# Optimization experiments

Measured on AMD Instinct MI355X. Metric: run time of the kernel, lower is better.

The kernel has to match this reference:

```python
import jax, jax.numpy as jnp
import numpy as np

PALACE_N = 64   # base palace mask size
PALACE_BLOCK = 8  # 8 palaces of 8 positions each


def _palace_base():
    # base 64x64 mask: 1.0 within a palace (8x8 diagonal blocks), 0.5 across palaces
    pid = jnp.arange(PALACE_N) // PALACE_BLOCK
    intra = pid[:, None] == pid[None, :]
    return jnp.where(intra, 1.0, 0.5).astype(jnp.float32)


def _get_mask(T, inter_palace_weight):
    # tile base mask by index modulo 64 (matches mask[i % 64, j % 64])
    base = _palace_base()
    ii = jnp.arange(T) % PALACE_N
    base_T = base[ii[:, None], ii[None, :]]            # [T, T]
    intra = (base_T == 1.0).astype(jnp.float32)
    inter = (base_T < 1.0).astype(jnp.float32)
    return intra + jax.nn.sigmoid(inter_palace_weight) * inter


def setup_inputs() -> dict:
    key = jax.random.key(0)
    ks = jax.random.split(key, 5)
    B, T, D = 4, 2048, 1024
    x = jax.random.normal(ks[0], (B, T, D), dtype=jnp.float32)
    s = 1.0 / np.sqrt(D)
    Wq = jax.random.normal(ks[1], (D, D), dtype=jnp.float32) * s
    Wk = jax.random.normal(ks[2], (D, D), dtype=jnp.float32) * s
    Wv = jax.random.normal(ks[3], (D, D), dtype=jnp.float32) * s
    inter_palace_weight = jnp.float32(0.1)
    return {"x": x, "Wq": Wq, "Wk": Wk, "Wv": Wv,
            "inter_palace_weight": inter_palace_weight}


def reference(x, Wq, Wk, Wv, inter_palace_weight):
    B, T, D = x.shape
    H = 16
    hd = D // H
    scale = hd ** -0.5
    pmask = _get_mask(T, inter_palace_weight)          # [T, T]
    # torch Linear: x @ W.T
    q = (x @ Wq.T).reshape(B, T, H, hd)
    k = (x @ Wk.T).reshape(B, T, H, hd)
    v = (x @ Wv.T).reshape(B, T, H, hd)
    attn = jnp.einsum('bqhd,bkhd->bhqk', q, k) * scale
    attn = attn * pmask[None, None, :, :]
    attn = jax.nn.softmax(attn, axis=-1)
    attn = jnp.nan_to_num(attn, nan=0.0)
    out = jnp.einsum('bhqk,bkhd->bqhd', attn, v)
    return out.reshape(B, T, D)
```

## Files before the change

kernel.cpp:

```cpp
#include <hip/hip_runtime.h>

typedef unsigned short u16;
typedef unsigned int u32;
typedef short bf16x8 __attribute__((ext_vector_type(8)));
typedef float f32x4 __attribute__((ext_vector_type(4)));

#define AS_GLOBAL __attribute__((address_space(1)))
#define AS_LDS __attribute__((address_space(3)))

__device__ __forceinline__ void async16(const void* g, void* l) {
  __builtin_amdgcn_global_load_lds((const AS_GLOBAL u32*)g, (AS_LDS u32*)l, 16, 0, 0);
}

__device__ __forceinline__ u16 f2bf(float f) {
  u32 u = __builtin_bit_cast(u32, f);
  u += 0x7FFFu + ((u >> 16) & 1u);
  return (u16)(u >> 16);
}

__device__ __forceinline__ u32 pk2bf(float lo, float hi) {
  return __builtin_amdgcn_perm(__builtin_bit_cast(u32, hi),
                               __builtin_bit_cast(u32, lo), 0x07060302u);
}

__device__ __forceinline__ float fexp2(float x) {
#if __has_builtin(__builtin_amdgcn_exp2f)
  return __builtin_amdgcn_exp2f(x);
#else
  return exp2f(x);
#endif
}

__global__ __launch_bounds__(256) void cvt_all(const float* __restrict__ x,
                                               const float* __restrict__ wq,
                                               const float* __restrict__ wk,
                                               const float* __restrict__ wv,
                                               u16* __restrict__ xb,
                                               u16* __restrict__ wb) {
  const int blk = blockIdx.x;
  const float* src;
  u16* dst;
  int i;
  if (blk < 8192) {
    src = x; dst = xb; i = blk * 256 + threadIdx.x;
  } else if (blk < 9216) {
    src = wq; dst = wb; i = (blk - 8192) * 256 + threadIdx.x;
  } else if (blk < 10240) {
    src = wk; dst = wb + 1048576; i = (blk - 9216) * 256 + threadIdx.x;
  } else {
    src = wv; dst = wb + 2097152; i = (blk - 10240) * 256 + threadIdx.x;
  }
  float4 f = reinterpret_cast<const float4*>(src)[i];
  ushort4 o;
  o.x = f2bf(f.x); o.y = f2bf(f.y); o.z = f2bf(f.z); o.w = f2bf(f.w);
  reinterpret_cast<ushort4*>(dst)[i] = o;
}

__global__ __launch_bounds__(256, 3) void qkv_gemm(const u16* __restrict__ X,
                                                   const u16* __restrict__ W,
                                                   u16* __restrict__ O) {
  const int z = blockIdx.z;
  const u16* Wz = W + (size_t)z * (1024 * 1024);
  u16* Oz = O + (size_t)z * (8192 * 1024);

  __shared__ __align__(16) u16 As[2][128 * 32];
  __shared__ __align__(16) u16 Bs[2][128 * 32];

  const int t = threadIdx.x;
  const int lane = t & 63, w = t >> 6, quad = lane >> 4, lq = lane & 15;
  const int wm = (w >> 1) * 64, wn = (w & 1) * 64;
  const size_t m0 = (size_t)blockIdx.x * 128;
  const int n0 = blockIdx.y * 128;
  const int srow = t >> 2, sseg = (t & 3) * 8;

  f32x4 acc[4][4];
#pragma unroll
  for (int i = 0; i < 4; ++i)
#pragma unroll
    for (int j = 0; j < 4; ++j) acc[i][j] = f32x4{0.f, 0.f, 0.f, 0.f};

  const u16* ga = X + (m0 + srow) * 1024 + sseg;
  const u16* gb = Wz + (size_t)(n0 + srow) * 1024 + sseg;

  async16(ga, &As[0][srow * 32 + sseg]);
  async16(ga + 64 * 1024, &As[0][(64 + srow) * 32 + sseg]);
  async16(gb, &Bs[0][srow * 32 + sseg]);
  async16(gb + 64 * 1024, &Bs[0][(64 + srow) * 32 + sseg]);

  for (int kt = 0; kt < 32; ++kt) {
    const int cur = kt & 1;
    __syncthreads();
    if (kt < 31) {
      const int k1 = (kt + 1) * 32;
      async16(ga + k1, &As[cur ^ 1][srow * 32 + sseg]);
      async16(ga + 64 * 1024 + k1, &As[cur ^ 1][(64 + srow) * 32 + sseg]);
      async16(gb + k1, &Bs[cur ^ 1][srow * 32 + sseg]);
      async16(gb + 64 * 1024 + k1, &Bs[cur ^ 1][(64 + srow) * 32 + sseg]);
    }
    bf16x8 af[4], bfr[4];
#pragma unroll
    for (int i = 0; i < 4; ++i)
      af[i] = *reinterpret_cast<const bf16x8*>(&As[cur][(wm + i * 16 + lq) * 32 + quad * 8]);
#pragma unroll
    for (int j = 0; j < 4; ++j)
      bfr[j] = *reinterpret_cast<const bf16x8*>(&Bs[cur][(wn + j * 16 + lq) * 32 + quad * 8]);
#pragma unroll
    for (int i = 0; i < 4; ++i)
#pragma unroll
      for (int j = 0; j < 4; ++j)
        acc[i][j] = __builtin_amdgcn_mfma_f32_16x16x32_bf16(af[i], bfr[j], acc[i][j], 0, 0, 0);
  }

#pragma unroll
  for (int i = 0; i < 4; ++i) {
#pragma unroll
    for (int j = 0; j < 4; ++j) {
      const int n = n0 + wn + j * 16 + lq;
      const int hh = n >> 6, d = n & 63;
#pragma unroll
      for (int r = 0; r < 4; ++r) {
        const size_t m = m0 + wm + i * 16 + quad * 4 + r;
        const size_t bb = m >> 11, tt = m & 2047;
        if (z != 2)
          Oz[((bb * 16 + hh) * 2048 + tt) * 64 + d] = f2bf(acc[i][j][r]);
        else
          Oz[((bb * 16 + hh) * 64 + d) * 2048 + tt] = f2bf(acc[i][j][r]);
      }
    }
  }
}

__global__ __launch_bounds__(256, 4) void palace_attn(const u16* __restrict__ Q,
                                                      const u16* __restrict__ K,
                                                      const u16* __restrict__ Vt,
                                                      float* __restrict__ out,
                                                      const float* __restrict__ wptr) {
  const int bh = blockIdx.x, qt = blockIdx.y;
  const int h = bh & 15, b = bh >> 4;
  const size_t base = (size_t)bh * (2048 * 64);

  __shared__ __align__(16) u16 Ks[64 * 64];
  __shared__ __align__(16) u16 Vs[64 * 64];
  __shared__ __align__(16) u16 Ps[4][32 * 72];

  const int t = threadIdx.x;
  const int w = t >> 6, lane = t & 63, quad = lane >> 4, lq = lane & 15;
  const float sig = 1.f / (1.f + __expf(-wptr[0]));
  const float Ci = 0.125f * 1.44269504f;
  const float Co = Ci * sig;
  const float MC = 14.4269504f;

  float coef[2][4];
#pragma unroll
  for (int qg = 0; qg < 2; ++qg) {
    const int qp = (((w & 1) * 32) + qg * 16 + lq) >> 3;
#pragma unroll
    for (int kg = 0; kg < 4; ++kg)
      coef[qg][kg] = (qp == kg * 2 + (quad >> 1)) ? Ci : Co;
  }

  bf16x8 qf[2][2];
#pragma unroll
  for (int qg = 0; qg < 2; ++qg)
#pragma unroll
    for (int kc = 0; kc < 2; ++kc)
      qf[qg][kc] = *reinterpret_cast<const bf16x8*>(
          Q + base + (size_t)(qt * 128 + w * 32 + qg * 16 + lq) * 64 + kc * 32 + quad * 8);

  int ko[2], vo[2];
#pragma unroll
  for (int r = 0; r < 2; ++r) {
    const int slot = r * 256 + t;
    const int row = slot >> 3;
    const int cl = (slot & 7) ^ (row & 7);
    ko[r] = row * 64 + cl * 8;
    vo[r] = row * 2048 + cl * 8;
  }

  f32x4 O[2][4];
  float lsum[2] = {0.f, 0.f};
#pragma unroll
  for (int qg = 0; qg < 2; ++qg)
#pragma unroll
    for (int dg = 0; dg < 4; ++dg) O[qg][dg] = f32x4{0.f, 0.f, 0.f, 0.f};

  const int x7 = lq & 7;

  for (int kt = 0; kt < 32; ++kt) {
    const u16* kgp = K + base + (size_t)kt * 4096;
    const u16* vgp = Vt + base + (size_t)kt * 64;
    __syncthreads();
    async16(kgp + ko[0], &Ks[(w * 64) * 8]);
    async16(kgp + ko[1], &Ks[(256 + w * 64) * 8]);
    async16(vgp + vo[0], &Vs[(w * 64) * 8]);
    async16(vgp + vo[1], &Vs[(256 + w * 64) * 8]);
    __syncthreads();

    f32x4 s[4][2];
#pragma unroll
    for (int kg = 0; kg < 4; ++kg) {
      const bf16x8 kf0 = *reinterpret_cast<const bf16x8*>(
          &Ks[(((kg * 16 + lq) * 8) + (quad ^ x7)) * 8]);
      const bf16x8 kf1 = *reinterpret_cast<const bf16x8*>(
          &Ks[(((kg * 16 + lq) * 8) + ((4 + quad) ^ x7)) * 8]);
#pragma unroll
      for (int qg = 0; qg < 2; ++qg) {
        f32x4 z = {0.f, 0.f, 0.f, 0.f};
        z = __builtin_amdgcn_mfma_f32_16x16x32_bf16(kf0, qf[qg][0], z, 0, 0, 0);
        s[kg][qg] = __builtin_amdgcn_mfma_f32_16x16x32_bf16(kf1, qf[qg][1], z, 0, 0, 0);
      }
    }

#pragma unroll
    for (int qg = 0; qg < 2; ++qg)
#pragma unroll
      for (int kg = 0; kg < 4; ++kg) {
        float p0 = fexp2(__builtin_fmaf(s[kg][qg][0], coef[qg][kg], -MC));
        float p1 = fexp2(__builtin_fmaf(s[kg][qg][1], coef[qg][kg], -MC));
        float p2 = fexp2(__builtin_fmaf(s[kg][qg][2], coef[qg][kg], -MC));
        float p3 = fexp2(__builtin_fmaf(s[kg][qg][3], coef[qg][kg], -MC));
        lsum[qg] += (p0 + p1) + (p2 + p3);
        uint2 pk;
        pk.x = pk2bf(p0, p1);
        pk.y = pk2bf(p2, p3);
        *reinterpret_cast<uint2*>(&Ps[w][(qg * 16 + lq) * 72 + kg * 16 + quad * 4]) = pk;
      }
    __asm__ volatile("s_waitcnt lgkmcnt(0)" ::: "memory");

    bf16x8 pf[2][2];
#pragma unroll
    for (int qg = 0; qg < 2; ++qg)
#pragma unroll
      for (int kc = 0; kc < 2; ++kc)
        pf[qg][kc] = *reinterpret_cast<const bf16x8*>(
            &Ps[w][(qg * 16 + lq) * 72 + kc * 32 + quad * 8]);

#pragma unroll
    for (int dg = 0; dg < 4; ++dg) {
      const bf16x8 vf0 = *reinterpret_cast<const bf16x8*>(
          &Vs[(((dg * 16 + lq) * 8) + (quad ^ x7)) * 8]);
      const bf16x8 vf1 = *reinterpret_cast<const bf16x8*>(
          &Vs[(((dg * 16 + lq) * 8) + ((4 + quad) ^ x7)) * 8]);
#pragma unroll
      for (int qg = 0; qg < 2; ++qg) {
        O[qg][dg] = __builtin_amdgcn_mfma_f32_16x16x32_bf16(pf[qg][0], vf0, O[qg][dg], 0, 0, 0);
        O[qg][dg] = __builtin_amdgcn_mfma_f32_16x16x32_bf16(pf[qg][1], vf1, O[qg][dg], 0, 0, 0);
      }
    }
  }

  float inv[2];
#pragma unroll
  for (int qg = 0; qg < 2; ++qg) {
    float l = lsum[qg];
    l += __shfl_xor(l, 16, 64);
    l += __shfl_xor(l, 32, 64);
    inv[qg] = 1.f / l;
  }

#pragma unroll
  for (int qg = 0; qg < 2; ++qg) {
#pragma unroll
    for (int r = 0; r < 4; ++r) {
      const float iv = __shfl(inv[qg], quad * 4 + r, 64);
      const size_t trow = (size_t)(qt * 128 + w * 32 + qg * 16 + quad * 4 + r);
      float* op = out + ((size_t)b * 2048 + trow) * 1024 + h * 64 + lq;
#pragma unroll
      for (int dg = 0; dg < 4; ++dg) op[dg * 16] = O[qg][dg][r] * iv;
    }
  }
}

extern "C" void kernel_launch(void* const* d_in, const int* in_sizes, int n_in,
                              void* d_out, int out_size, void* d_ws, size_t ws_size,
                              hipStream_t stream) {
  (void)in_sizes; (void)n_in; (void)out_size; (void)ws_size;
  const float* x = (const float*)d_in[0];
  const float* Wq = (const float*)d_in[1];
  const float* Wk = (const float*)d_in[2];
  const float* Wv = (const float*)d_in[3];
  const float* wip = (const float*)d_in[4];
  float* out = (float*)d_out;

  u16* xb = (u16*)d_ws;
  u16* wb = xb + 8388608;
  u16* qb = wb + 3145728;
  u16* kb = qb + 8388608;
  u16* vb = kb + 8388608;

  cvt_all<<<11264, 256, 0, stream>>>(x, Wq, Wk, Wv, xb, wb);
  qkv_gemm<<<dim3(64, 8, 3), 256, 0, stream>>>(xb, wb, qb);
  palace_attn<<<dim3(64, 16, 1), 256, 0, stream>>>(qb, kb, vb, out, wip);
}
```

Before: 260.9 us.

## Double-buffer K/V tiles and double query rows per wave in palace attention

The attention kernel now processes 64 query rows per wave (256 per block), halving the grid, so each K/V tile loaded into LDS is reused across twice as many queries. K and V tiles are double-buffered, with the next tile's async loads issued before the current tile is computed, which removes one barrier per iteration. The P scratch layout switches from padded rows to an XOR swizzle, and the mask coefficient is computed per diagonal block. The costs are more registers (occupancy bound drops to 2), more LDS, and fewer blocks in flight.

```diff
diff --git a/kernel.cpp b/kernel.cpp
--- a/kernel.cpp
+++ b/kernel.cpp
@@ -130,7 +130,7 @@
   }
 }
 
-__global__ __launch_bounds__(256, 4) void palace_attn(const u16* __restrict__ Q,
+__global__ __launch_bounds__(256, 2) void palace_attn(const u16* __restrict__ Q,
                                                       const u16* __restrict__ K,
                                                       const u16* __restrict__ Vt,
                                                       float* __restrict__ out,
@@ -139,33 +139,27 @@
   const int h = bh & 15, b = bh >> 4;
   const size_t base = (size_t)bh * (2048 * 64);
 
-  __shared__ __align__(16) u16 Ks[64 * 64];
-  __shared__ __align__(16) u16 Vs[64 * 64];
-  __shared__ __align__(16) u16 Ps[4][32 * 72];
+  __shared__ __align__(16) u16 Ks[2][64 * 64];
+  __shared__ __align__(16) u16 Vs[2][64 * 64];
+  __shared__ __align__(16) u16 Ps[4][64 * 64];
 
   const int t = threadIdx.x;
   const int w = t >> 6, lane = t & 63, quad = lane >> 4, lq = lane & 15;
+  const int q1 = quad >> 1, q0 = quad & 1, x7 = lq & 7;
   const float sig = 1.f / (1.f + __expf(-wptr[0]));
   const float Ci = 0.125f * 1.44269504f;
   const float Co = Ci * sig;
   const float MC = 14.4269504f;
 
-  float coef[2][4];
-#pragma unroll
-  for (int qg = 0; qg < 2; ++qg) {
-    const int qp = (((w & 1) * 32) + qg * 16 + lq) >> 3;
-#pragma unroll
-    for (int kg = 0; kg < 4; ++kg)
-      coef[qg][kg] = (qp == kg * 2 + (quad >> 1)) ? Ci : Co;
-  }
-
-  bf16x8 qf[2][2];
-#pragma unroll
-  for (int qg = 0; qg < 2; ++qg)
+  const float Cd = ((lq >> 3) == q1) ? Ci : Co;
+
+  bf16x8 qf[4][2];
+#pragma unroll
+  for (int qg = 0; qg < 4; ++qg)
 #pragma unroll
     for (int kc = 0; kc < 2; ++kc)
       qf[qg][kc] = *reinterpret_cast<const bf16x8*>(
-          Q + base + (size_t)(qt * 128 + w * 32 + qg * 16 + lq) * 64 + kc * 32 + quad * 8);
+          Q + base + (size_t)(qt * 256 + w * 64 + qg * 16 + lq) * 64 + kc * 32 + quad * 8);
 
   int ko[2], vo[2];
 #pragma unroll
@@ -177,81 +171,86 @@
     vo[r] = row * 2048 + cl * 8;
   }
 
-  f32x4 O[2][4];
-  float lsum[2] = {0.f, 0.f};
-#pragma unroll
-  for (int qg = 0; qg < 2; ++qg)
+  f32x4 O[4][4];
+  float lsum[4] = {0.f, 0.f, 0.f, 0.f};
+#pragma unroll
+  for (int qg = 0; qg < 4; ++qg)
 #pragma unroll
     for (int dg = 0; dg < 4; ++dg) O[qg][dg] = f32x4{0.f, 0.f, 0.f, 0.f};
 
-  const int x7 = lq & 7;
+  {
+    const u16* kgp = K + base;
+    const u16* vgp = Vt + base;
+    async16(kgp + ko[0], &Ks[0][(w * 64) * 8]);
+    async16(kgp + ko[1], &Ks[0][(256 + w * 64) * 8]);
+    async16(vgp + vo[0], &Vs[0][(w * 64) * 8]);
+    async16(vgp + vo[1], &Vs[0][(256 + w * 64) * 8]);
+  }
 
   for (int kt = 0; kt < 32; ++kt) {
-    const u16* kgp = K + base + (size_t)kt * 4096;
-    const u16* vgp = Vt + base + (size_t)kt * 64;
+    const int cur = kt & 1;
     __syncthreads();
-    async16(kgp + ko[0], &Ks[(w * 64) * 8]);
-    async16(kgp + ko[1], &Ks[(256 + w * 64) * 8]);
-    async16(vgp + vo[0], &Vs[(w * 64) * 8]);
-    async16(vgp + vo[1], &Vs[(256 + w * 64) * 8]);
-    __syncthreads();
-
-    f32x4 s[4][2];
+    if (kt < 31) {
+      const u16* kgp = K + base + (size_t)(kt + 1) * 4096;
+      const u16* vgp = Vt + base + (size_t)(kt + 1) * 64;
+      const int nb = cur ^ 1;
+      async16(kgp + ko[0], &Ks[nb][(w * 64) * 8]);
+      async16(kgp + ko[1], &Ks[nb][(256 + w * 64) * 8]);
+      async16(vgp + vo[0], &Vs[nb][(w * 64) * 8]);
+      async16(vgp + vo[1], &Vs[nb][(256 + w * 64) * 8]);
+    }
+
 #pragma unroll
     for (int kg = 0; kg < 4; ++kg) {
       const bf16x8 kf0 = *reinterpret_cast<const bf16x8*>(
-          &Ks[(((kg * 16 + lq) * 8) + (quad ^ x7)) * 8]);
+          &Ks[cur][((kg * 16 + lq) * 8 + (quad ^ x7)) * 8]);
       const bf16x8 kf1 = *reinterpret_cast<const bf16x8*>(
-          &Ks[(((kg * 16 + lq) * 8) + ((4 + quad) ^ x7)) * 8]);
-#pragma unroll
-      for (int qg = 0; qg < 2; ++qg) {
+          &Ks[cur][((kg * 16 + lq) * 8 + ((4 + quad) ^ x7)) * 8]);
+      f32x4 s[4];
+#pragma unroll
+      for (int qg = 0; qg < 4; ++qg) {
         f32x4 z = {0.f, 0.f, 0.f, 0.f};
         z = __builtin_amdgcn_mfma_f32_16x16x32_bf16(kf0, qf[qg][0], z, 0, 0, 0);
-        s[kg][qg] = __builtin_amdgcn_mfma_f32_16x16x32_bf16(kf1, qf[qg][1], z, 0, 0, 0);
-      }
-    }
-
-#pragma unroll
-    for (int qg = 0; qg < 2; ++qg)
-#pragma unroll
-      for (int kg = 0; kg < 4; ++kg) {
-        float p0 = fexp2(__builtin_fmaf(s[kg][qg][0], coef[qg][kg], -MC));
-        float p1 = fexp2(__builtin_fmaf(s[kg][qg][1], coef[qg][kg], -MC));
-        float p2 = fexp2(__builtin_fmaf(s[kg][qg][2], coef[qg][kg], -MC));
-        float p3 = fexp2(__builtin_fmaf(s[kg][qg][3], coef[qg][kg], -MC));
+        s[qg] = __builtin_amdgcn_mfma_f32_16x16x32_bf16(kf1, qf[qg][1], z, 0, 0, 0);
+      }
+      const int pchunk = ((kg * 2 + q1) ^ x7) * 8 + q0 * 4;
+#pragma unroll
+      for (int qg = 0; qg < 4; ++qg) {
+        const float cf = (kg == qg) ? Cd : Co;
+        float p0 = fexp2(__builtin_fmaf(s[qg][0], cf, -MC));
+        float p1 = fexp2(__builtin_fmaf(s[qg][1], cf, -MC));
+        float p2 = fexp2(__builtin_fmaf(s[qg][2], cf, -MC));
+        float p3 = fexp2(__builtin_fmaf(s[qg][3], cf, -MC));
         lsum[qg] += (p0 + p1) + (p2 + p3);
         uint2 pk;
         pk.x = pk2bf(p0, p1);
         pk.y = pk2bf(p2, p3);
-        *reinterpret_cast<uint2*>(&Ps[w][(qg * 16 + lq) * 72 + kg * 16 + quad * 4]) = pk;
-      }
+        *reinterpret_cast<uint2*>(&Ps[w][(qg * 16 + lq) * 64 + pchunk]) = pk;
+      }
+    }
     __asm__ volatile("s_waitcnt lgkmcnt(0)" ::: "memory");
-
-    bf16x8 pf[2][2];
-#pragma unroll
-    for (int qg = 0; qg < 2; ++qg)
-#pragma unroll
-      for (int kc = 0; kc < 2; ++kc)
-        pf[qg][kc] = *reinterpret_cast<const bf16x8*>(
-            &Ps[w][(qg * 16 + lq) * 72 + kc * 32 + quad * 8]);
 
 #pragma unroll
     for (int dg = 0; dg < 4; ++dg) {
       const bf16x8 vf0 = *reinterpret_cast<const bf16x8*>(
-          &Vs[(((dg * 16 + lq) * 8) + (quad ^ x7)) * 8]);
+          &Vs[cur][((dg * 16 + lq) * 8 + (quad ^ x7)) * 8]);
       const bf16x8 vf1 = *reinterpret_cast<const bf16x8*>(
-          &Vs[(((dg * 16 + lq) * 8) + ((4 + quad) ^ x7)) * 8]);
-#pragma unroll
-      for (int qg = 0; qg < 2; ++qg) {
-        O[qg][dg] = __builtin_amdgcn_mfma_f32_16x16x32_bf16(pf[qg][0], vf0, O[qg][dg], 0, 0, 0);
-        O[qg][dg] = __builtin_amdgcn_mfma_f32_16x16x32_bf16(pf[qg][1], vf1, O[qg][dg], 0, 0, 0);
-      }
-    }
-  }
-
-  float inv[2];
-#pragma unroll
-  for (int qg = 0; qg < 2; ++qg) {
+          &Vs[cur][((dg * 16 + lq) * 8 + ((4 + quad) ^ x7)) * 8]);
+#pragma unroll
+      for (int qg = 0; qg < 4; ++qg) {
+        const bf16x8 pf0 = *reinterpret_cast<const bf16x8*>(
+            &Ps[w][(qg * 16 + lq) * 64 + ((quad) ^ x7) * 8]);
+        const bf16x8 pf1 = *reinterpret_cast<const bf16x8*>(
+            &Ps[w][(qg * 16 + lq) * 64 + ((4 + quad) ^ x7) * 8]);
+        O[qg][dg] = __builtin_amdgcn_mfma_f32_16x16x32_bf16(pf0, vf0, O[qg][dg], 0, 0, 0);
+        O[qg][dg] = __builtin_amdgcn_mfma_f32_16x16x32_bf16(pf1, vf1, O[qg][dg], 0, 0, 0);
+      }
+    }
+  }
+
+  float inv[4];
+#pragma unroll
+  for (int qg = 0; qg < 4; ++qg) {
     float l = lsum[qg];
     l += __shfl_xor(l, 16, 64);
     l += __shfl_xor(l, 32, 64);
@@ -259,11 +258,11 @@
   }
 
 #pragma unroll
-  for (int qg = 0; qg < 2; ++qg) {
+  for (int qg = 0; qg < 4; ++qg) {
 #pragma unroll
     for (int r = 0; r < 4; ++r) {
       const float iv = __shfl(inv[qg], quad * 4 + r, 64);
-      const size_t trow = (size_t)(qt * 128 + w * 32 + qg * 16 + quad * 4 + r);
+      const size_t trow = (size_t)(qt * 256 + w * 64 + qg * 16 + quad * 4 + r);
       float* op = out + ((size_t)b * 2048 + trow) * 1024 + h * 64 + lq;
 #pragma unroll
       for (int dg = 0; dg < 4; ++dg) op[dg * 16] = O[qg][dg][r] * iv;
@@ -290,5 +289,5 @@
 
   cvt_all<<<11264, 256, 0, stream>>>(x, Wq, Wk, Wv, xb, wb);
   qkv_gemm<<<dim3(64, 8, 3), 256, 0, stream>>>(xb, wb, qb);
-  palace_attn<<<dim3(64, 16, 1), 256, 0, stream>>>(qb, kb, vb, out, wip);
-}
+  palace_attn<<<dim3(64, 8, 1), 256, 0, stream>>>(qb, kb, vb, out, wip);
+}
```

Measured after the change: 265.5 us. Within noise of the previous version (+1.7%).
